# Kernel tuning notes

Measured on AMD Instinct MI355X. Metric: run time of the kernel, lower is better.

The kernel has to match this reference:

```python
import jax, jax.numpy as jnp
import numpy as np

N, DEG, FIN, HID, OUT = 50000, 16, 128, 128, 64


def setup_inputs() -> dict:
    key = jax.random.key(0)
    ks = jax.random.split(key, 32)
    x = jax.random.normal(ks[0], (N, FIN), dtype=jnp.float32)
    src = jax.random.randint(ks[1], (N * DEG,), 0, N, dtype=jnp.int32)
    dst = jnp.repeat(jnp.arange(N, dtype=jnp.int32), DEG)  # sorted by target, fixed degree
    edge_index = jnp.stack([src, dst])  # [2, E]
    dims = [(FIN, HID), (HID, HID), (HID, OUT)]
    params = {}
    i = 2
    for l, (fi, fo) in enumerate(dims, 1):
        s_lstm = 1.0 / np.sqrt(fi)
        params[f"W_ih{l}"] = jax.random.normal(ks[i + 0], (4 * fi, fi)) * s_lstm
        params[f"W_hh{l}"] = jax.random.normal(ks[i + 1], (4 * fi, fi)) * s_lstm
        params[f"b_ih{l}"] = jax.random.normal(ks[i + 2], (4 * fi,)) * s_lstm
        params[f"b_hh{l}"] = jax.random.normal(ks[i + 3], (4 * fi,)) * s_lstm
        params[f"Wl{l}"] = jax.random.normal(ks[i + 4], (fo, fi)) * (1.0 / np.sqrt(fi))
        params[f"bl{l}"] = jnp.zeros((fo,), jnp.float32)
        params[f"Wr{l}"] = jax.random.normal(ks[i + 5], (fo, fi)) * (1.0 / np.sqrt(fi))
        i += 6
    return {"x": x, "edge_index": edge_index, **params}


def _lstm_last(neigh, Wih, Whh, bih, bhh):
    # neigh: [N, deg, Fi]; PyTorch LSTM gate order i,f,g,o; return last-step output h.
    h0 = jnp.zeros((neigh.shape[0], Wih.shape[0] // 4), neigh.dtype)
    bias = bih + bhh

    def step(carry, xt):
        h, c = carry
        g = xt @ Wih.T + h @ Whh.T + bias
        i, f, gg, o = jnp.split(g, 4, axis=-1)
        c = jax.nn.sigmoid(f) * c + jax.nn.sigmoid(i) * jnp.tanh(gg)
        h = jax.nn.sigmoid(o) * jnp.tanh(c)
        return (h, c), None

    (h, _), _ = jax.lax.scan(step, (h0, h0), jnp.swapaxes(neigh, 0, 1))
    return h


def _sage_layer(x, src2d, Wih, Whh, bih, bhh, Wl, bl, Wr):
    neigh = x[src2d]  # gather: [N, deg, Fi]
    aggr = _lstm_last(neigh, Wih, Whh, bih, bhh)  # [N, Fi]
    return aggr @ Wl.T + bl + x @ Wr.T  # lin_l(aggr) + lin_r(x)


def reference(x, edge_index,
              W_ih1, W_hh1, b_ih1, b_hh1, Wl1, bl1, Wr1,
              W_ih2, W_hh2, b_ih2, b_hh2, Wl2, bl2, Wr2,
              W_ih3, W_hh3, b_ih3, b_hh3, Wl3, bl3, Wr3):
    n = x.shape[0]
    src2d = edge_index[0].reshape(n, -1)  # fixed-degree, dst-sorted edge list
    h = _sage_layer(x, src2d, W_ih1, W_hh1, b_ih1, b_hh1, Wl1, bl1, Wr1)
    h = jax.nn.relu(h)  # dropout is identity in eval mode
    h = _sage_layer(h, src2d, W_ih2, W_hh2, b_ih2, b_hh2, Wl2, bl2, Wr2)
    h = jax.nn.relu(h)
    return _sage_layer(h, src2d, W_ih3, W_hh3, b_ih3, b_hh3, Wl3, bl3, Wr3)
```

## Files before the change

### kernel.cpp

```cpp
#include <hip/hip_runtime.h>
#include <cstddef>
#include <cstdint>

typedef __attribute__((ext_vector_type(4))) float f32x4;
typedef __attribute__((ext_vector_type(8))) short short8;

#define HID 128
#define NK1 -1.4426950408889634f
#define PK2 2.8853900817779268f

#define BAR_LGKM() __asm__ volatile("s_waitcnt lgkmcnt(0)\ns_barrier" ::: "memory")
#define STEP_BAR2() __asm__ volatile("s_waitcnt vmcnt(2) lgkmcnt(0)\ns_barrier" ::: "memory")
#define BAR_VM_LGKM() __asm__ volatile("s_waitcnt vmcnt(0) lgkmcnt(0)\ns_barrier" ::: "memory")

__device__ __forceinline__ short f2bf(float f) {
  unsigned u = __builtin_bit_cast(unsigned, f);
  u += 0x7FFFu + ((u >> 16) & 1u);
  return (short)(u >> 16);
}
__device__ __forceinline__ unsigned pack_bf2(float a, float b) {
  unsigned ua = __builtin_bit_cast(unsigned, a) + 0x8000u;
  unsigned ub = __builtin_bit_cast(unsigned, b) + 0x8000u;
  return __builtin_amdgcn_perm(ub, ua, 0x07060302u);
}

__device__ __forceinline__ float lstm_elem(float si, float sf, float sg, float so, float& c) {
  float Ei = __builtin_amdgcn_exp2f(si);
  float Ef = __builtin_amdgcn_exp2f(sf);
  float Tg = __builtin_amdgcn_exp2f(sg);
  float Eo = __builtin_amdgcn_exp2f(so);
  float u = 1.0f + Ei, w = 1.0f + Ef, v = Tg + 1.0f, Tm = Tg - 1.0f;
  float t0 = u * v;
  float num = __builtin_fmaf(c, t0, w * Tm);
  float cn = num * __builtin_amdgcn_rcpf(w * t0);
  c = cn;
  float Tc = __builtin_amdgcn_exp2f(PK2 * cn);
  return (Tc - 1.0f) * __builtin_amdgcn_rcpf((1.0f + Eo) * (Tc + 1.0f));
}

struct ConvParams {
  const float* x; short* xb; int n;
  const float* Wih[3]; const float* Whh[3];
  const float* bih[3]; const float* bhh[3];
  const float* Wl[3];  const float* Wr[3];
  short* wihB[3]; short* whhB[3]; short* wlB[3]; short* wrB[3];
  float* bsum[3];
  int foK[3];
  int* tctr;
};

__global__ void conv_all_kernel(ConvParams p) {
  const int gi = blockIdx.x * blockDim.x + threadIdx.x;
  const int gs = gridDim.x * blockDim.x;
  if (gi < 8) p.tctr[gi] = 0;
  for (int i = gi; i < p.n; i += gs) p.xb[i] = f2bf(p.x[i]);
#pragma unroll 1
  for (int l = 0; l < 3; ++l) {
    if (gi < 512 * HID) {
      float sc = ((gi >> 14) == 2) ? PK2 : NK1;
      p.wihB[l][gi] = f2bf(p.Wih[l][gi] * sc);
      p.whhB[l][gi] = f2bf(p.Whh[l][gi] * sc);
    }
    if (gi < p.foK[l]) {
      p.wlB[l][gi] = f2bf(p.Wl[l][gi]);
      p.wrB[l][gi] = f2bf(p.Wr[l][gi]);
    }
    if (gi < 512)
      p.bsum[l][gi] = (p.bih[l][gi] + p.bhh[l][gi]) * (((gi >> 7) == 2) ? PK2 : NK1);
  }
}

#define OSTR 524
#define ASTR 136
__global__ __launch_bounds__(512, 4) void pgemm_kernel(
    const short* __restrict__ A, const short* __restrict__ W,
    const float* __restrict__ bias, short* __restrict__ out, int M, int ntiles) {
  __shared__ short ldsA[32 * ASTR];
  __shared__ short ldsO[32 * OSTR];
  const int tid = threadIdx.x;
  const int wave = tid >> 6, lane = tid & 63;
  const int quad = lane >> 4, nn = lane & 15;
  const int cbase = wave * 64;

  short8 wreg[4][4];
#pragma unroll
  for (int kt = 0; kt < 4; ++kt)
#pragma unroll
    for (int nt = 0; nt < 4; ++nt)
      wreg[kt][nt] = *(const short8*)(W + (size_t)(cbase + nt * 16 + nn) * HID + kt * 32 + quad * 8);
  f32x4 bias4[4];
#pragma unroll
  for (int nt = 0; nt < 4; ++nt)
#pragma unroll
    for (int r = 0; r < 4; ++r) bias4[nt][r] = bias[cbase + nt * 16 + quad * 4 + r];

  const int srow = wave * 4 + quad;
  const int scol = nn * 8;

#pragma unroll 1
  for (int rt = blockIdx.x; rt < ntiles; rt += gridDim.x) {
    const int row0 = rt * 32;
    {
      int r = row0 + srow;
      if (r > M - 1) r = M - 1;
      short8 av = *(const short8*)(A + (size_t)r * HID + scol);
      *(short8*)(ldsA + srow * ASTR + scol) = av;
    }
    BAR_VM_LGKM();

    f32x4 acc[2][4];
#pragma unroll
    for (int b = 0; b < 2; ++b)
#pragma unroll
      for (int nt = 0; nt < 4; ++nt) acc[b][nt] = bias4[nt];
#pragma unroll
    for (int kt = 0; kt < 4; ++kt) {
      short8 af0 = *(const short8*)(ldsA + nn * ASTR + kt * 32 + quad * 8);
      short8 af1 = *(const short8*)(ldsA + (16 + nn) * ASTR + kt * 32 + quad * 8);
#pragma unroll
      for (int nt = 0; nt < 4; ++nt) {
        acc[0][nt] = __builtin_amdgcn_mfma_f32_16x16x32_bf16(wreg[kt][nt], af0, acc[0][nt], 0, 0, 0);
        acc[1][nt] = __builtin_amdgcn_mfma_f32_16x16x32_bf16(wreg[kt][nt], af1, acc[1][nt], 0, 0, 0);
      }
    }
    BAR_LGKM();
#pragma unroll
    for (int b = 0; b < 2; ++b)
#pragma unroll
      for (int nt = 0; nt < 4; ++nt) {
        uint2 pk;
        pk.x = pack_bf2(acc[b][nt][0], acc[b][nt][1]);
        pk.y = pack_bf2(acc[b][nt][2], acc[b][nt][3]);
        *(uint2*)(ldsO + (b * 16 + nn) * OSTR + cbase + nt * 16 + quad * 4) = pk;
      }
    BAR_LGKM();
#pragma unroll
    for (int idx = tid; idx < 32 * 64; idx += 512) {
      int row = idx >> 6, c8 = (idx & 63) * 8;
      if (row0 + row < M)
        *(short8*)(out + (size_t)(row0 + row) * 512 + c8) = *(const short8*)(ldsO + row * OSTR + c8);
    }
  }
}

#define NPB 16
#define PSTR 520
#define HSTR 152
#define LSTM_LDS_BYTES ((3 * NPB * PSTR + 2 * NPB * HSTR) * 2 + 256 * 4 + 16)

template <int FO, bool RELU, bool OUTF32>
__global__ __launch_bounds__(512, 4) void lstm_fused_kernel(
    const short* __restrict__ P, const short* __restrict__ Whh,
    const int* __restrict__ src, const short* __restrict__ cur,
    const short* __restrict__ Wl, const short* __restrict__ Wr,
    const float* __restrict__ bl,
    short* __restrict__ outB, float* __restrict__ outF, int M, int ntiles,
    int* __restrict__ tctr) {
  extern __shared__ char smem[];
  short* Pb = (short*)smem;
  short* Hb = Pb + 3 * NPB * PSTR;
  int* srcL = (int*)(Hb + 2 * NPB * HSTR);
  int* nextTp = srcL + 256;

  const int tid = threadIdx.x;
  const int wave = tid >> 6, lane = tid & 63;
  const int quad = lane >> 4, nn = lane & 15;
  const int r0row = wave * 2, r1row = wave * 2 + 1;
  const char* Pbase = (const char*)P + lane * 16;

  short8 wreg[4][4];
#pragma unroll
  for (int kt = 0; kt < 4; ++kt)
#pragma unroll
    for (int q = 0; q < 4; ++q)
      wreg[kt][q] = *(const short8*)(Whh + (size_t)(q * 128 + wave * 16 + nn) * HID + kt * 32 + quad * 8);

  short8 ident;
#pragma unroll
  for (int e = 0; e < 8; ++e) ident[e] = (short)((quad * 8 + e == nn) ? 0x3F80 : 0);
  f32x4 zero4 = {0.f, 0.f, 0.f, 0.f};
  __asm__ volatile("" : "+v"(zero4));

  int tile = blockIdx.x;
  while (tile < ntiles) {
    const int nodeBase = tile * NPB;
    if (tid < 256) {
      int node = nodeBase + (tid >> 4);
      srcL[tid] = ((node < M) ? src[nodeBase * 16 + tid] : 0) << 10;
    }
    if (tid == 0) *nextTp = (int)gridDim.x + atomicAdd(tctr, 1);
    float c_st[4] = {0.f, 0.f, 0.f, 0.f};
    BAR_LGKM();
    const int my_next = *nextTp;

    {
      int s0A = srcL[r0row * 16 + 0], s0B = srcL[r1row * 16 + 0];
      __builtin_amdgcn_global_load_lds(
          (const __attribute__((address_space(1))) unsigned int*)(Pbase + s0A),
          (__attribute__((address_space(3))) unsigned int*)(Pb + r0row * PSTR), 16, 0, 0);
      __builtin_amdgcn_global_load_lds(
          (const __attribute__((address_space(1))) unsigned int*)(Pbase + s0B),
          (__attribute__((address_space(3))) unsigned int*)(Pb + r1row * PSTR), 16, 0, 0);
      int s1A = srcL[r0row * 16 + 1], s1B = srcL[r1row * 16 + 1];
      __builtin_amdgcn_global_load_lds(
          (const __attribute__((address_space(1))) unsigned int*)(Pbase + s1A),
          (__attribute__((address_space(3))) unsigned int*)(Pb + NPB * PSTR + r0row * PSTR), 16, 0, 0);
      __builtin_amdgcn_global_load_lds(
          (const __attribute__((address_space(1))) unsigned int*)(Pbase + s1B),
          (__attribute__((address_space(3))) unsigned int*)(Pb + NPB * PSTR + r1row * PSTR), 16, 0, 0);
    }
    int sA = srcL[r0row * 16 + 2], sB = srcL[r1row * 16 + 2];

    int pc = 0, pg = 2;
#pragma unroll 1
    for (int t = 0; t < 16; ++t) {
      short* Pc = Pb + pc * NPB * PSTR;
      short* Pg = Pb + pg * NPB * PSTR;
      const short* Hp = Hb + ((t + 1) & 1) * NPB * HSTR;
      short* Hw = Hb + (t & 1) * NPB * HSTR;
      pc = (pc == 2) ? 0 : pc + 1;
      pg = (pg == 2) ? 0 : pg + 1;

      STEP_BAR2();

      const short* pB = Pc + nn * PSTR + wave * 16 + (quad & 1) * 8;
      short8 pf0 = *(const short8*)(pB + 0 * 128);
      short8 pf1 = *(const short8*)(pB + 1 * 128);
      short8 pf2 = *(const short8*)(pB + 2 * 128);
      short8 pf3 = *(const short8*)(pB + 3 * 128);

      __builtin_amdgcn_global_load_lds(
          (const __attribute__((address_space(1))) unsigned int*)(Pbase + sA),
          (__attribute__((address_space(3))) unsigned int*)(Pg + r0row * PSTR), 16, 0, 0);
      __builtin_amdgcn_global_load_lds(
          (const __attribute__((address_space(1))) unsigned int*)(Pbase + sB),
          (__attribute__((address_space(3))) unsigned int*)(Pg + r1row * PSTR), 16, 0, 0);
      {
        int tn = (t + 3 < 16) ? t + 3 : 15;
        sA = srcL[r0row * 16 + tn];
        sB = srcL[r1row * 16 + tn];
      }

      f32x4 acc[4];
      acc[0] = __builtin_amdgcn_mfma_f32_16x16x32_bf16(ident, pf0, zero4, 0, 0, 0);
      acc[1] = __builtin_amdgcn_mfma_f32_16x16x32_bf16(ident, pf1, zero4, 0, 0, 0);
      acc[2] = __builtin_amdgcn_mfma_f32_16x16x32_bf16(ident, pf2, zero4, 0, 0, 0);
      acc[3] = __builtin_amdgcn_mfma_f32_16x16x32_bf16(ident, pf3, zero4, 0, 0, 0);

      if (t) {
#pragma unroll
        for (int kt = 0; kt < 4; ++kt) {
          short8 hb = *(const short8*)(Hp + nn * HSTR + kt * 32 + quad * 8);
#pragma unroll
          for (int q = 0; q < 4; ++q)
            acc[q] = __builtin_amdgcn_mfma_f32_16x16x32_bf16(wreg[kt][q], hb, acc[q], 0, 0, 0);
        }
      }

      float hv[4];
#pragma unroll
      for (int r = 0; r < 4; ++r)
        hv[r] = lstm_elem(acc[0][r], acc[1][r], acc[2][r], acc[3][r], c_st[r]);
      uint2 pk;
      pk.x = pack_bf2(hv[0], hv[1]);
      pk.y = pack_bf2(hv[2], hv[3]);
      *(uint2*)(Hw + nn * HSTR + wave * 16 + quad * 4) = pk;
    }

    BAR_LGKM();

    if (FO == 128 || wave < 4) {
      const short* Hf = Hb + NPB * HSTR;
      const int cbase = wave * 16;
      f32x4 accO;
#pragma unroll
      for (int r = 0; r < 4; ++r) accO[r] = bl[cbase + quad * 4 + r];
#pragma unroll
      for (int kt = 0; kt < 4; ++kt) {
        short8 wlA = *(const short8*)(Wl + (size_t)(cbase + nn) * HID + kt * 32 + quad * 8);
        short8 hb = *(const short8*)(Hf + nn * HSTR + kt * 32 + quad * 8);
        accO = __builtin_amdgcn_mfma_f32_16x16x32_bf16(wlA, hb, accO, 0, 0, 0);
        short8 wrA = *(const short8*)(Wr + (size_t)(cbase + nn) * HID + kt * 32 + quad * 8);
        short8 cb = *(const short8*)(cur + (size_t)(nodeBase + nn) * HID + kt * 32 + quad * 8);
        accO = __builtin_amdgcn_mfma_f32_16x16x32_bf16(wrA, cb, accO, 0, 0, 0);
      }
      if (RELU) {
#pragma unroll
        for (int r = 0; r < 4; ++r) accO[r] = fmaxf(accO[r], 0.0f);
      }
      int node = nodeBase + nn;
      if (node < M) {
        if (OUTF32) {
          *(f32x4*)(outF + (size_t)node * FO + cbase + quad * 4) = accO;
        } else {
          uint2 pko;
          pko.x = pack_bf2(accO[0], accO[1]);
          pko.y = pack_bf2(accO[2], accO[3]);
          *(uint2*)(outB + (size_t)node * FO + cbase + quad * 4) = pko;
        }
      }
    }
    tile = my_next;
  }
}

extern "C" void kernel_launch(void* const* d_in, const int* in_sizes, int n_in,
                              void* d_out, int out_size, void* d_ws, size_t ws_size,
                              hipStream_t stream) {
  const float* x = (const float*)d_in[0];
  const int* src = (const int*)d_in[1];
  const float* Wih[3] = {(const float*)d_in[2], (const float*)d_in[9], (const float*)d_in[16]};
  const float* Whh[3] = {(const float*)d_in[3], (const float*)d_in[10], (const float*)d_in[17]};
  const float* bih[3] = {(const float*)d_in[4], (const float*)d_in[11], (const float*)d_in[18]};
  const float* bhh[3] = {(const float*)d_in[5], (const float*)d_in[12], (const float*)d_in[19]};
  const float* Wl[3]  = {(const float*)d_in[6], (const float*)d_in[13], (const float*)d_in[20]};
  const float* bl[3]  = {(const float*)d_in[7], (const float*)d_in[14], (const float*)d_in[21]};
  const float* Wr[3]  = {(const float*)d_in[8], (const float*)d_in[15], (const float*)d_in[22]};

  const int M = in_sizes[0] / HID;

  char* ws = (char*)d_ws;
  size_t off = 0;
  auto alloc = [&](size_t bytes) -> void* {
    void* p = ws + off;
    off += (bytes + 255) & ~(size_t)255;
    return p;
  };
  short* curA = (short*)alloc((size_t)M * HID * 2);
  short* curB = (short*)alloc((size_t)M * HID * 2);
  short* Pbuf = (short*)alloc((size_t)M * 512 * 2);
  short* wihB[3]; short* whhB[3]; short* wlB[3]; short* wrB[3]; float* bsum[3];
  for (int l = 0; l < 3; ++l) {
    wihB[l] = (short*)alloc(512 * HID * 2);
    whhB[l] = (short*)alloc(512 * HID * 2);
    wlB[l]  = (short*)alloc(HID * HID * 2);
    wrB[l]  = (short*)alloc(HID * HID * 2);
    bsum[l] = (float*)alloc(512 * 4);
  }
  int* tctr = (int*)alloc(256);

  const int nltiles = (M + NPB - 1) / NPB;
  const int ntiles = (M + 31) / 32;

  (void)hipFuncSetAttribute((const void*)lstm_fused_kernel<128, true, false>,
                            hipFuncAttributeMaxDynamicSharedMemorySize, LSTM_LDS_BYTES);
  (void)hipFuncSetAttribute((const void*)lstm_fused_kernel<64, false, true>,
                            hipFuncAttributeMaxDynamicSharedMemorySize, LSTM_LDS_BYTES);

  ConvParams cp;
  cp.x = x; cp.xb = curA; cp.n = M * HID; cp.tctr = tctr;
  for (int l = 0; l < 3; ++l) {
    cp.Wih[l] = Wih[l]; cp.Whh[l] = Whh[l];
    cp.bih[l] = bih[l]; cp.bhh[l] = bhh[l];
    cp.Wl[l] = Wl[l];   cp.Wr[l] = Wr[l];
    cp.wihB[l] = wihB[l]; cp.whhB[l] = whhB[l];
    cp.wlB[l] = wlB[l];   cp.wrB[l] = wrB[l];
    cp.bsum[l] = bsum[l];
    cp.foK[l] = ((l == 2) ? 64 : 128) * HID;
  }
  conv_all_kernel<<<2048, 256, 0, stream>>>(cp);

  short* cur = curA;
  short* nxt = curB;
  for (int l = 0; l < 3; ++l) {
    pgemm_kernel<<<784, 512, 0, stream>>>(cur, wihB[l], bsum[l], Pbuf, M, ntiles);
    if (l < 2) {
      lstm_fused_kernel<128, true, false><<<512, 512, LSTM_LDS_BYTES, stream>>>(
          Pbuf, whhB[l], src, cur, wlB[l], wrB[l], bl[l], nxt, nullptr, M, nltiles, tctr + l);
      short* tswap = cur; cur = nxt; nxt = tswap;
    } else {
      lstm_fused_kernel<64, false, true><<<512, 512, LSTM_LDS_BYTES, stream>>>(
          Pbuf, whhB[l], src, cur, wlB[l], wrB[l], bl[l], nullptr, (float*)d_out, M, nltiles,
          tctr + 2);
    }
  }
}
```

Before: 704.0 us.

## Fuse next layer's input-projection GEMM into the LSTM kernel epilogue

The LSTM kernel for layers 1 and 2 now stages its bf16 output tile in shared memory. It then multiplies that tile by the next layer's W_ih and adds the bias sum, writing the gate pre-activations straight into a second P buffer. This removes two standalone pgemm launches and the extra global read of the layer activations they needed. In exchange, each 16-node tile reloads a full 512x128 W_ih slice from L2 and reuses the P staging area in shared memory as scratch, which adds load traffic and may race with prefetching of the next tile. A fallback path keeps the old schedule when the workspace is too small for the second P buffer.

```diff
diff --git a/kernel.cpp b/kernel.cpp
--- a/kernel.cpp
+++ b/kernel.cpp
@@ -148,14 +148,15 @@
 #define HSTR 152
 #define LSTM_LDS_BYTES ((3 * NPB * PSTR + 2 * NPB * HSTR) * 2 + 256 * 4 + 16)
 
-template <int FO, bool RELU, bool OUTF32>
+template <int FO, bool RELU, bool OUTF32, bool FUSEP>
 __global__ __launch_bounds__(512, 4) void lstm_fused_kernel(
     const short* __restrict__ P, const short* __restrict__ Whh,
     const int* __restrict__ src, const short* __restrict__ cur,
     const short* __restrict__ Wl, const short* __restrict__ Wr,
     const float* __restrict__ bl,
-    short* __restrict__ outB, float* __restrict__ outF, int M, int ntiles,
-    int* __restrict__ tctr) {
+    short* __restrict__ outB, float* __restrict__ outF,
+    const short* __restrict__ WihN, const float* __restrict__ bsumN,
+    short* __restrict__ Pnext, int M, int ntiles, int* __restrict__ tctr) {
   extern __shared__ char smem[];
   short* Pb = (short*)smem;
   short* Hb = Pb + 3 * NPB * PSTR;
@@ -289,14 +290,45 @@
         for (int r = 0; r < 4; ++r) accO[r] = fmaxf(accO[r], 0.0f);
       }
       int node = nodeBase + nn;
+      uint2 pko;
+      pko.x = pack_bf2(accO[0], accO[1]);
+      pko.y = pack_bf2(accO[2], accO[3]);
       if (node < M) {
         if (OUTF32) {
           *(f32x4*)(outF + (size_t)node * FO + cbase + quad * 4) = accO;
         } else {
-          uint2 pko;
-          pko.x = pack_bf2(accO[0], accO[1]);
-          pko.y = pack_bf2(accO[2], accO[3]);
           *(uint2*)(outB + (size_t)node * FO + cbase + quad * 4) = pko;
+        }
+      }
+      if (FUSEP) {
+        *(uint2*)(Pb + nn * ASTR + cbase + quad * 4) = pko;
+      }
+    }
+
+    if (FUSEP) {
+      BAR_LGKM();
+      const int pbase = wave * 64;
+      f32x4 pacc[4];
+#pragma unroll
+      for (int nt = 0; nt < 4; ++nt)
+        pacc[nt] = *(const f32x4*)(bsumN + pbase + nt * 16 + quad * 4);
+#pragma unroll
+      for (int kt = 0; kt < 4; ++kt) {
+        short8 ob = *(const short8*)(Pb + nn * ASTR + kt * 32 + quad * 8);
+#pragma unroll
+        for (int nt = 0; nt < 4; ++nt) {
+          short8 wf = *(const short8*)(WihN + (size_t)(pbase + nt * 16 + nn) * HID + kt * 32 + quad * 8);
+          pacc[nt] = __builtin_amdgcn_mfma_f32_16x16x32_bf16(wf, ob, pacc[nt], 0, 0, 0);
+        }
+      }
+      int node = nodeBase + nn;
+      if (node < M) {
+#pragma unroll
+        for (int nt = 0; nt < 4; ++nt) {
+          uint2 pk2;
+          pk2.x = pack_bf2(pacc[nt][0], pacc[nt][1]);
+          pk2.y = pack_bf2(pacc[nt][2], pacc[nt][3]);
+          *(uint2*)(Pnext + (size_t)node * 512 + pbase + nt * 16 + quad * 4) = pk2;
         }
       }
     }
@@ -328,7 +360,7 @@
   };
   short* curA = (short*)alloc((size_t)M * HID * 2);
   short* curB = (short*)alloc((size_t)M * HID * 2);
-  short* Pbuf = (short*)alloc((size_t)M * 512 * 2);
+  short* PbufA = (short*)alloc((size_t)M * 512 * 2);
   short* wihB[3]; short* whhB[3]; short* wlB[3]; short* wrB[3]; float* bsum[3];
   for (int l = 0; l < 3; ++l) {
     wihB[l] = (short*)alloc(512 * HID * 2);
@@ -339,12 +371,18 @@
   }
   int* tctr = (int*)alloc(256);
 
+  const size_t pbytes = ((size_t)M * 512 * 2 + 255) & ~(size_t)255;
+  const bool fused = (off + pbytes) <= ws_size;
+  short* PbufB = fused ? (short*)alloc((size_t)M * 512 * 2) : nullptr;
+
   const int nltiles = (M + NPB - 1) / NPB;
   const int ntiles = (M + 31) / 32;
 
-  (void)hipFuncSetAttribute((const void*)lstm_fused_kernel<128, true, false>,
+  (void)hipFuncSetAttribute((const void*)lstm_fused_kernel<128, true, false, true>,
                             hipFuncAttributeMaxDynamicSharedMemorySize, LSTM_LDS_BYTES);
-  (void)hipFuncSetAttribute((const void*)lstm_fused_kernel<64, false, true>,
+  (void)hipFuncSetAttribute((const void*)lstm_fused_kernel<128, true, false, false>,
+                            hipFuncAttributeMaxDynamicSharedMemorySize, LSTM_LDS_BYTES);
+  (void)hipFuncSetAttribute((const void*)lstm_fused_kernel<64, false, true, false>,
                             hipFuncAttributeMaxDynamicSharedMemorySize, LSTM_LDS_BYTES);
 
   ConvParams cp;
@@ -360,18 +398,32 @@
   }
   conv_all_kernel<<<2048, 256, 0, stream>>>(cp);
 
-  short* cur = curA;
-  short* nxt = curB;
-  for (int l = 0; l < 3; ++l) {
-    pgemm_kernel<<<784, 512, 0, stream>>>(cur, wihB[l], bsum[l], Pbuf, M, ntiles);
-    if (l < 2) {
-      lstm_fused_kernel<128, true, false><<<512, 512, LSTM_LDS_BYTES, stream>>>(
-          Pbuf, whhB[l], src, cur, wlB[l], wrB[l], bl[l], nxt, nullptr, M, nltiles, tctr + l);
-      short* tswap = cur; cur = nxt; nxt = tswap;
-    } else {
-      lstm_fused_kernel<64, false, true><<<512, 512, LSTM_LDS_BYTES, stream>>>(
-          Pbuf, whhB[l], src, cur, wlB[l], wrB[l], bl[l], nullptr, (float*)d_out, M, nltiles,
-          tctr + 2);
-    }
-  }
-}
+  if (fused) {
+    pgemm_kernel<<<784, 512, 0, stream>>>(curA, wihB[0], bsum[0], PbufA, M, ntiles);
+    lstm_fused_kernel<128, true, false, true><<<512, 512, LSTM_LDS_BYTES, stream>>>(
+        PbufA, whhB[0], src, curA, wlB[0], wrB[0], bl[0], curB, nullptr,
+        wihB[1], bsum[1], PbufB, M, nltiles, tctr + 0);
+    lstm_fused_kernel<128, true, false, true><<<512, 512, LSTM_LDS_BYTES, stream>>>(
+        PbufB, whhB[1], src, curB, wlB[1], wrB[1], bl[1], curA, nullptr,
+        wihB[2], bsum[2], PbufA, M, nltiles, tctr + 1);
+    lstm_fused_kernel<64, false, true, false><<<512, 512, LSTM_LDS_BYTES, stream>>>(
+        PbufA, whhB[2], src, curA, wlB[2], wrB[2], bl[2], nullptr, (float*)d_out,
+        nullptr, nullptr, nullptr, M, nltiles, tctr + 2);
+  } else {
+    short* cur = curA;
+    short* nxt = curB;
+    for (int l = 0; l < 3; ++l) {
+      pgemm_kernel<<<784, 512, 0, stream>>>(cur, wihB[l], bsum[l], PbufA, M, ntiles);
+      if (l < 2) {
+        lstm_fused_kernel<128, true, false, false><<<512, 512, LSTM_LDS_BYTES, stream>>>(
+            PbufA, whhB[l], src, cur, wlB[l], wrB[l], bl[l], nxt, nullptr,
+            nullptr, nullptr, nullptr, M, nltiles, tctr + l);
+        short* tswap = cur; cur = nxt; nxt = tswap;
+      } else {
+        lstm_fused_kernel<64, false, true, false><<<512, 512, LSTM_LDS_BYTES, stream>>>(
+            PbufA, whhB[l], src, cur, wlB[l], wrB[l], bl[l], nullptr, (float*)d_out,
+            nullptr, nullptr, nullptr, M, nltiles, tctr + 2);
+      }
+    }
+  }
+}
```

Result: slower. 773.4 us (+9.9%).
